# Optimization experiments

Hardware: AMD Instinct MI355X
Metric: run time of the kernel (lower is better)

The kernel has to match this reference:

```python
import jax, jax.numpy as jnp
import numpy as np

SIZE = 8192            # size_kernel
HALF = SIZE // 2       # 4096, output dim of k/q/v projections
N = 4096               # sequence length; must equal HALF for the elementwise combine
SCALE = float(int(SIZE ** 0.5))  # source does int(size**0.5) -> 90, not sqrt(8192)


def setup_inputs() -> dict:
    key = jax.random.key(0)
    ks = jax.random.split(key, 7)
    s = 0.02
    x = jax.random.normal(ks[0], (N, SIZE), dtype=jnp.float32)
    Wk = jax.random.normal(ks[1], (SIZE, HALF), dtype=jnp.float32) * s
    bk = jnp.zeros((HALF,), dtype=jnp.float32)
    Wv = jax.random.normal(ks[2], (SIZE, HALF), dtype=jnp.float32) * s
    bv = jnp.zeros((HALF,), dtype=jnp.float32)
    Wq = jax.random.normal(ks[3], (SIZE, HALF), dtype=jnp.float32) * s
    bq = jnp.zeros((HALF,), dtype=jnp.float32)
    return {"x": x, "Wk": Wk, "bk": bk, "Wv": Wv, "bv": bv, "Wq": Wq, "bq": bq}


def reference(x, Wk, bk, Wv, bv, Wq, bq):
    # faithful to source: query layer exists but x_q = self.value(x) (bug kept)
    x_k = x @ Wk + bk                      # [N, HALF]
    x_v = x @ Wv + bv                      # [N, HALF]
    x_q = x @ Wv + bv                      # [N, HALF]  (uses value weights, as in source)
    scores = (x_q @ x_k.T) / SCALE         # [N, N]
    att = jax.nn.softmax(scores, axis=-1)  # [N, N]
    result = att * x_v                     # elementwise combine (N == HALF)
    vals = jnp.max(result, axis=1)         # [N]
    idx = jnp.argmax(result, axis=1)       # [N] int
    return vals, idx
```

## Files before the change

### kernel.cpp

```cpp
#include <hip/hip_runtime.h>
#include <math.h>

typedef _Float16 half8 __attribute__((ext_vector_type(8)));
typedef float f32x4 __attribute__((ext_vector_type(4)));

#define BM 128
#define BN 64
#define BK 64
#define LO_SCALE 2048.0f
#define INV_LO_SCALE (1.0f / 2048.0f)

__device__ __forceinline__ void f16split(float a, _Float16& hi, _Float16& lo) {
    hi = (_Float16)a;
    float r = a - (float)hi;
    lo = (_Float16)(r * LO_SCALE);
}

__device__ __forceinline__ void glds16(const void* g, void* l) {
    __builtin_amdgcn_global_load_lds(
        (const __attribute__((address_space(1))) unsigned int*)g,
        (__attribute__((address_space(3))) unsigned int*)l, 16, 0, 0);
}

__global__ __launch_bounds__(256, 3) void gemm_nt_split(
    const _Float16* __restrict__ A0, const _Float16* __restrict__ A1,
    const _Float16* __restrict__ B0, const _Float16* __restrict__ B1,
    float* __restrict__ C, int K, const float* __restrict__ bias)
{
    __shared__ _Float16 lds[24576];
    char* lb = (char*)&lds[0];
    const int tid = threadIdx.x;
    const int w = tid >> 6, l = tid & 63;
    const int br = blockIdx.y * BM, bc = blockIdx.x * BN;

    f32x4 acc1[4][2], acc2[4][2];
    const f32x4 zero = {0.f, 0.f, 0.f, 0.f};
    #pragma unroll
    for (int m = 0; m < 4; ++m)
        #pragma unroll
        for (int n = 0; n < 2; ++n) { acc1[m][n] = zero; acc2[m][n] = zero; }

    const int srow = tid >> 3;
    const int cg   = (tid & 7) ^ ((tid >> 3) & 7);
    const _Float16* pA0 = A0 + (size_t)(br + srow) * K + cg * 8;
    const _Float16* pA1 = A1 + (size_t)(br + srow) * K + cg * 8;
    const _Float16* pB0 = B0 + (size_t)(bc + srow) * K + cg * 8;
    const _Float16* pB1 = B1 + (size_t)(bc + srow) * K + cg * 8;
    const size_t rstep = (size_t)32 * K;

    const int so = tid * 16;

    const int fr = l & 15, fq = l >> 4;
    const int arow0 = (w >> 1) * 64;
    const int bcol0 = (w & 1) * 32;
    const int cs0 = (((0 * 4) + fq) ^ (fr & 7)) * 16;
    const int cs1 = (((1 * 4) + fq) ^ (fr & 7)) * 16;

    for (int k0 = 0; k0 < K; k0 += BK) {
        __syncthreads();
        glds16(pA0,             lb + 0     + so);
        glds16(pA0 + rstep,     lb + 4096  + so);
        glds16(pA0 + 2 * rstep, lb + 8192  + so);
        glds16(pA0 + 3 * rstep, lb + 12288 + so);
        glds16(pA1,             lb + 16384 + so);
        glds16(pA1 + rstep,     lb + 20480 + so);
        glds16(pA1 + 2 * rstep, lb + 24576 + so);
        glds16(pA1 + 3 * rstep, lb + 28672 + so);
        glds16(pB0,             lb + 32768 + so);
        glds16(pB0 + rstep,     lb + 36864 + so);
        glds16(pB1,             lb + 40960 + so);
        glds16(pB1 + rstep,     lb + 45056 + so);
        pA0 += BK; pA1 += BK; pB0 += BK; pB1 += BK;
        __syncthreads();

        #pragma unroll
        for (int s = 0; s < 2; ++s) {
            const int cs = s ? cs1 : cs0;
            half8 ah[4], al[4], bh[2], bl[2];
            #pragma unroll
            for (int m = 0; m < 4; ++m) {
                const int roff = (arow0 + m * 16 + fr) * 128 + cs;
                ah[m] = *(const half8*)(lb + 0     + roff);
                al[m] = *(const half8*)(lb + 16384 + roff);
            }
            #pragma unroll
            for (int n = 0; n < 2; ++n) {
                const int roff = (bcol0 + n * 16 + fr) * 128 + cs;
                bh[n] = *(const half8*)(lb + 32768 + roff);
                bl[n] = *(const half8*)(lb + 40960 + roff);
            }
            #pragma unroll
            for (int m = 0; m < 4; ++m)
                #pragma unroll
                for (int n = 0; n < 2; ++n) {
                    acc1[m][n] = __builtin_amdgcn_mfma_f32_16x16x32_f16(ah[m], bh[n], acc1[m][n], 0, 0, 0);
                    acc2[m][n] = __builtin_amdgcn_mfma_f32_16x16x32_f16(ah[m], bl[n], acc2[m][n], 0, 0, 0);
                    acc2[m][n] = __builtin_amdgcn_mfma_f32_16x16x32_f16(al[m], bh[n], acc2[m][n], 0, 0, 0);
                }
        }
    }

    float bb[2];
    const bool has_bias = (bias != nullptr);
    #pragma unroll
    for (int n = 0; n < 2; ++n)
        bb[n] = has_bias ? bias[bc + bcol0 + n * 16 + fr] : 0.0f;

    #pragma unroll
    for (int m = 0; m < 4; ++m) {
        const int row0 = br + arow0 + m * 16 + fq * 4;
        #pragma unroll
        for (int n = 0; n < 2; ++n) {
            const int col = bc + bcol0 + n * 16 + fr;
            #pragma unroll
            for (int q = 0; q < 4; ++q) {
                float v = acc1[m][n][q] + acc2[m][n][q] * INV_LO_SCALE;
                v = has_bias ? (v + bb[n]) : (v / 90.0f);
                C[(size_t)(row0 + q) * 4096 + col] = v;
            }
        }
    }
}

__global__ __launch_bounds__(256) void split2(const float* __restrict__ X,
                                              _Float16* __restrict__ H,
                                              _Float16* __restrict__ L,
                                              long n4)
{
    long i = (long)blockIdx.x * 256 + threadIdx.x;
    const long stride = (long)gridDim.x * 256;
    for (; i < n4; i += stride) {
        float4 v = ((const float4*)X)[i];
        float xs[4] = {v.x, v.y, v.z, v.w};
        _Float16 hh[4], ll[4];
        #pragma unroll
        for (int e = 0; e < 4; ++e) f16split(xs[e], hh[e], ll[e]);
        typedef _Float16 half4v __attribute__((ext_vector_type(4)));
        half4v hv = {hh[0], hh[1], hh[2], hh[3]};
        half4v lv = {ll[0], ll[1], ll[2], ll[3]};
        ((half4v*)H)[i] = hv;
        ((half4v*)L)[i] = lv;
    }
}

__global__ __launch_bounds__(256) void splitT(const float* __restrict__ W,
                                              _Float16* __restrict__ HT,
                                              _Float16* __restrict__ LT,
                                              int R, int Ccols)
{
    __shared__ float t[64][65];
    const int tid = threadIdx.x;
    const int rb = blockIdx.y * 64, cb = blockIdx.x * 64;
    #pragma unroll
    for (int i = 0; i < 4; ++i) {
        const int row = i * 16 + (tid >> 4);
        const int col = (tid & 15) * 4;
        float4 v = *(const float4*)&W[(size_t)(rb + row) * Ccols + cb + col];
        t[row][col] = v.x; t[row][col + 1] = v.y;
        t[row][col + 2] = v.z; t[row][col + 3] = v.w;
    }
    __syncthreads();
    #pragma unroll
    for (int i = 0; i < 2; ++i) {
        const int oc = i * 32 + (tid >> 3);
        const int r8 = (tid & 7) * 8;
        half8 hv, lv;
        #pragma unroll
        for (int e = 0; e < 8; ++e) {
            _Float16 hb, lb2;
            f16split(t[r8 + e][oc], hb, lb2);
            hv[e] = hb; lv[e] = lb2;
        }
        const size_t o = (size_t)(cb + oc) * R + rb + r8;
        *(half8*)&HT[o] = hv;
        *(half8*)&LT[o] = lv;
    }
}

__global__ __launch_bounds__(256) void row_reduce(const float* __restrict__ S,
                                                  const float* __restrict__ XV,
                                                  float* __restrict__ out)
{
    const int row = blockIdx.x;
    const float* s  = S  + (size_t)row * 4096;
    const float* xv = XV + (size_t)row * 4096;
    const int tid = threadIdx.x;
    __shared__ float red[256];
    __shared__ int   redi[256];

    float m = -INFINITY;
    for (int j = tid; j < 4096; j += 256) m = fmaxf(m, s[j]);
    red[tid] = m;
    __syncthreads();
    for (int st = 128; st > 0; st >>= 1) {
        if (tid < st) red[tid] = fmaxf(red[tid], red[tid + st]);
        __syncthreads();
    }
    m = red[0];
    __syncthreads();

    float z = 0.f;
    for (int j = tid; j < 4096; j += 256) z += expf(s[j] - m);
    red[tid] = z;
    __syncthreads();
    for (int st = 128; st > 0; st >>= 1) {
        if (tid < st) red[tid] += red[tid + st];
        __syncthreads();
    }
    const float Z = red[0];
    __syncthreads();

    float best = -INFINITY;
    int bidx = 0x7fffffff;
    for (int j = tid; j < 4096; j += 256) {
        float att = expf(s[j] - m) / Z;
        float p = att * xv[j];
        if (p > best) { best = p; bidx = j; }
    }
    red[tid] = best; redi[tid] = bidx;
    __syncthreads();
    for (int st = 128; st > 0; st >>= 1) {
        if (tid < st) {
            float v2 = red[tid + st]; int i2 = redi[tid + st];
            if (v2 > red[tid] || (v2 == red[tid] && i2 < redi[tid])) {
                red[tid] = v2; redi[tid] = i2;
            }
        }
        __syncthreads();
    }
    if (tid == 0) {
        out[row]        = red[0];
        out[4096 + row] = (float)redi[0];
    }
}

extern "C" void kernel_launch(void* const* d_in, const int* in_sizes, int n_in,
                              void* d_out, int out_size, void* d_ws, size_t ws_size,
                              hipStream_t stream) {
    (void)in_sizes; (void)n_in; (void)out_size; (void)d_ws; (void)ws_size;
    const float* x  = (const float*)d_in[0];
    const float* Wk = (const float*)d_in[1];
    const float* bk = (const float*)d_in[2];
    const float* Wv = (const float*)d_in[3];
    const float* bv = (const float*)d_in[4];

    _Float16* xs0 = (_Float16*)d_in[5];
    _Float16* xs1 = xs0 + 33554432UL;
    _Float16* wT0 = (_Float16*)d_in[0];
    _Float16* wT1 = wT0 + 33554432UL;
    float* xk = (float*)d_in[1];
    float* xv = (float*)d_in[3];
    _Float16* k0s = (_Float16*)d_in[5];
    _Float16* k1s = k0s + 16777216UL;
    _Float16* v0s = k1s + 16777216UL;
    _Float16* v1s = v0s + 16777216UL;
    float* S = (float*)d_in[0];

    dim3 blk(256);
    dim3 g(4096 / BN, 4096 / BM);
    split2<<<2048, blk, 0, stream>>>(x, xs0, xs1, (long)(4096UL * 8192UL / 4UL));
    splitT<<<dim3(64, 128), blk, 0, stream>>>(Wk, wT0, wT1, 8192, 4096);
    gemm_nt_split<<<g, blk, 0, stream>>>(xs0, xs1, wT0, wT1, xk, 8192, bk);
    splitT<<<dim3(64, 128), blk, 0, stream>>>(Wv, wT0, wT1, 8192, 4096);
    gemm_nt_split<<<g, blk, 0, stream>>>(xs0, xs1, wT0, wT1, xv, 8192, bv);
    split2<<<2048, blk, 0, stream>>>(xk, k0s, k1s, (long)(4096UL * 4096UL / 4UL));
    split2<<<2048, blk, 0, stream>>>(xv, v0s, v1s, (long)(4096UL * 4096UL / 4UL));
    gemm_nt_split<<<g, blk, 0, stream>>>(v0s, v1s, k0s, k1s, S, 4096, nullptr);
    row_reduce<<<4096, 256, 0, stream>>>(S, xv, (float*)d_out);
}
```

Before: 2.498 ms.

## Double-buffer split-fp16 GEMM with 512-thread 128x128 tiles and XCD swizzle

The split-precision GEMM now uses 128x128 tiles with 8 waves and two LDS buffers. Global-to-LDS loads for tile t+2 are issued while tile t is computed, using explicit vmcnt waits and barriers instead of a full sync each iteration. A block-index swizzle groups neighbouring tiles per XCD for L2 reuse, and MFMA sections run at raised wave priority. The 128 KB of LDS limits occupancy, and the hand-written waitcnt counts are fragile.

```diff
diff --git a/kernel.cpp b/kernel.cpp
--- a/kernel.cpp
+++ b/kernel.cpp
@@ -5,7 +5,7 @@
 typedef float f32x4 __attribute__((ext_vector_type(4)));
 
 #define BM 128
-#define BN 64
+#define BN 128
 #define BK 64
 #define LO_SCALE 2048.0f
 #define INV_LO_SCALE (1.0f / 2048.0f)
@@ -22,16 +22,22 @@
         (__attribute__((address_space(3))) unsigned int*)l, 16, 0, 0);
 }
 
-__global__ __launch_bounds__(256, 3) void gemm_nt_split(
+__global__ __launch_bounds__(512, 2) void gemm_nt_split(
     const _Float16* __restrict__ A0, const _Float16* __restrict__ A1,
     const _Float16* __restrict__ B0, const _Float16* __restrict__ B1,
     float* __restrict__ C, int K, const float* __restrict__ bias)
 {
-    __shared__ _Float16 lds[24576];
-    char* lb = (char*)&lds[0];
+    __shared__ _Float16 lds[2][32768];
     const int tid = threadIdx.x;
     const int w = tid >> 6, l = tid & 63;
-    const int br = blockIdx.y * BM, bc = blockIdx.x * BN;
+
+    const int nbx = gridDim.x;
+    const int flat = blockIdx.y * nbx + blockIdx.x;
+    const int nwg = nbx * gridDim.y;
+    const int cpx = nwg >> 3;
+    const int swz = (flat & 7) * cpx + (flat >> 3);
+    const int bxs = swz % nbx, bys = swz / nbx;
+    const int br = bys * BM, bc = bxs * BN;
 
     f32x4 acc1[4][2], acc2[4][2];
     const f32x4 zero = {0.f, 0.f, 0.f, 0.f};
@@ -41,37 +47,47 @@
         for (int n = 0; n < 2; ++n) { acc1[m][n] = zero; acc2[m][n] = zero; }
 
     const int srow = tid >> 3;
-    const int cg   = (tid & 7) ^ ((tid >> 3) & 7);
-    const _Float16* pA0 = A0 + (size_t)(br + srow) * K + cg * 8;
-    const _Float16* pA1 = A1 + (size_t)(br + srow) * K + cg * 8;
-    const _Float16* pB0 = B0 + (size_t)(bc + srow) * K + cg * 8;
-    const _Float16* pB1 = B1 + (size_t)(bc + srow) * K + cg * 8;
-    const size_t rstep = (size_t)32 * K;
-
+    const int cg   = (tid & 7) ^ (srow & 7);
+    const _Float16* gA0 = A0 + (size_t)(br + srow) * K + cg * 8;
+    const _Float16* gA1 = A1 + (size_t)(br + srow) * K + cg * 8;
+    const _Float16* gB0 = B0 + (size_t)(bc + srow) * K + cg * 8;
+    const _Float16* gB1 = B1 + (size_t)(bc + srow) * K + cg * 8;
+    const size_t r64 = (size_t)64 * K;
     const int so = tid * 16;
 
+    char* lb0 = (char*)&lds[0][0];
+    char* lb1 = (char*)&lds[1][0];
+
+    auto stage = [&](char* lb, int kt) {
+        const size_t ko = (size_t)kt * BK;
+        glds16(gA0 + ko,       lb + 0     + so);
+        glds16(gA0 + ko + r64, lb + 8192  + so);
+        glds16(gA1 + ko,       lb + 16384 + so);
+        glds16(gA1 + ko + r64, lb + 24576 + so);
+        glds16(gB0 + ko,       lb + 32768 + so);
+        glds16(gB0 + ko + r64, lb + 40960 + so);
+        glds16(gB1 + ko,       lb + 49152 + so);
+        glds16(gB1 + ko + r64, lb + 57344 + so);
+    };
+
     const int fr = l & 15, fq = l >> 4;
-    const int arow0 = (w >> 1) * 64;
-    const int bcol0 = (w & 1) * 32;
+    const int arow0 = (w >> 2) * 64;
+    const int bcol0 = (w & 3) * 32;
     const int cs0 = (((0 * 4) + fq) ^ (fr & 7)) * 16;
     const int cs1 = (((1 * 4) + fq) ^ (fr & 7)) * 16;
 
-    for (int k0 = 0; k0 < K; k0 += BK) {
-        __syncthreads();
-        glds16(pA0,             lb + 0     + so);
-        glds16(pA0 + rstep,     lb + 4096  + so);
-        glds16(pA0 + 2 * rstep, lb + 8192  + so);
-        glds16(pA0 + 3 * rstep, lb + 12288 + so);
-        glds16(pA1,             lb + 16384 + so);
-        glds16(pA1 + rstep,     lb + 20480 + so);
-        glds16(pA1 + 2 * rstep, lb + 24576 + so);
-        glds16(pA1 + 3 * rstep, lb + 28672 + so);
-        glds16(pB0,             lb + 32768 + so);
-        glds16(pB0 + rstep,     lb + 36864 + so);
-        glds16(pB1,             lb + 40960 + so);
-        glds16(pB1 + rstep,     lb + 45056 + so);
-        pA0 += BK; pA1 += BK; pB0 += BK; pB1 += BK;
-        __syncthreads();
+    const int nt = K / BK;
+    stage(lb0, 0);
+    stage(lb1, 1);
+
+    for (int t = 0; t < nt; ++t) {
+        char* lb = (t & 1) ? lb1 : lb0;
+        if (t < nt - 1) {
+            asm volatile("s_waitcnt vmcnt(8)" ::: "memory");
+        } else {
+            asm volatile("s_waitcnt vmcnt(0)" ::: "memory");
+        }
+        asm volatile("s_barrier" ::: "memory");
 
         #pragma unroll
         for (int s = 0; s < 2; ++s) {
@@ -87,8 +103,9 @@
             for (int n = 0; n < 2; ++n) {
                 const int roff = (bcol0 + n * 16 + fr) * 128 + cs;
                 bh[n] = *(const half8*)(lb + 32768 + roff);
-                bl[n] = *(const half8*)(lb + 40960 + roff);
-            }
+                bl[n] = *(const half8*)(lb + 49152 + roff);
+            }
+            __builtin_amdgcn_s_setprio(1);
             #pragma unroll
             for (int m = 0; m < 4; ++m)
                 #pragma unroll
@@ -97,7 +114,12 @@
                     acc2[m][n] = __builtin_amdgcn_mfma_f32_16x16x32_f16(ah[m], bl[n], acc2[m][n], 0, 0, 0);
                     acc2[m][n] = __builtin_amdgcn_mfma_f32_16x16x32_f16(al[m], bh[n], acc2[m][n], 0, 0, 0);
                 }
-        }
+            __builtin_amdgcn_s_setprio(0);
+        }
+
+        asm volatile("s_waitcnt lgkmcnt(0)" ::: "memory");
+        asm volatile("s_barrier" ::: "memory");
+        if (t + 2 < nt) stage(lb, t + 2);
     }
 
     float bb[2];
@@ -256,15 +278,16 @@
     _Float16* v1s = v0s + 16777216UL;
     float* S = (float*)d_in[0];
 
-    dim3 blk(256);
+    dim3 blk(512);
     dim3 g(4096 / BN, 4096 / BM);
-    split2<<<2048, blk, 0, stream>>>(x, xs0, xs1, (long)(4096UL * 8192UL / 4UL));
-    splitT<<<dim3(64, 128), blk, 0, stream>>>(Wk, wT0, wT1, 8192, 4096);
+    dim3 sblk(256);
+    split2<<<2048, sblk, 0, stream>>>(x, xs0, xs1, (long)(4096UL * 8192UL / 4UL));
+    splitT<<<dim3(64, 128), sblk, 0, stream>>>(Wk, wT0, wT1, 8192, 4096);
     gemm_nt_split<<<g, blk, 0, stream>>>(xs0, xs1, wT0, wT1, xk, 8192, bk);
-    splitT<<<dim3(64, 128), blk, 0, stream>>>(Wv, wT0, wT1, 8192, 4096);
+    splitT<<<dim3(64, 128), sblk, 0, stream>>>(Wv, wT0, wT1, 8192, 4096);
     gemm_nt_split<<<g, blk, 0, stream>>>(xs0, xs1, wT0, wT1, xv, 8192, bv);
-    split2<<<2048, blk, 0, stream>>>(xk, k0s, k1s, (long)(4096UL * 4096UL / 4UL));
-    split2<<<2048, blk, 0, stream>>>(xv, v0s, v1s, (long)(4096UL * 4096UL / 4UL));
+    split2<<<2048, sblk, 0, stream>>>(xk, k0s, k1s, (long)(4096UL * 4096UL / 4UL));
+    split2<<<2048, sblk, 0, stream>>>(xv, v0s, v1s, (long)(4096UL * 4096UL / 4UL));
     gemm_nt_split<<<g, blk, 0, stream>>>(v0s, v1s, k0s, k1s, S, 4096, nullptr);
     row_reduce<<<4096, 256, 0, stream>>>(S, xv, (float*)d_out);
 }
```

Measured after the change: 2.847 ms. 1.14x slower.
